# Optimization experiments

Measured on AMD Instinct MI355X. Metric: run time of the kernel, lower is better.

## Reference

```python
import jax, jax.numpy as jnp
import numpy as np

B, IN, E, H, V, MAX_LEN = 512, 64, 512, 1024, 1024, 32
LN_EPS = 1e-5


def setup_inputs() -> dict:
    key = jax.random.key(0)
    ks = jax.random.split(key, 16)
    s = 0.02
    n = lambda k, shp: jax.random.normal(k, shp, jnp.float32) * s
    return {
        "x": jax.random.normal(ks[0], (B, IN), jnp.float32),
        "w_in": n(ks[1], (E, IN)), "b_in": jnp.zeros((E,), jnp.float32),
        "w_ih0": n(ks[2], (4 * H, E)), "w_hh0": n(ks[3], (4 * H, H)),
        "b_ih0": jnp.zeros((4 * H,), jnp.float32), "b_hh0": jnp.zeros((4 * H,), jnp.float32),
        "w_ih1": n(ks[4], (4 * H, H)), "w_hh1": n(ks[5], (4 * H, H)),
        "b_ih1": jnp.zeros((4 * H,), jnp.float32), "b_hh1": jnp.zeros((4 * H,), jnp.float32),
        "ln_g": jnp.ones((H,), jnp.float32), "ln_b": jnp.zeros((H,), jnp.float32),
        "w_out": n(ks[6], (V, H)), "b_out": jnp.zeros((V,), jnp.float32),
        "emb": n(ks[7], (V, E)),
    }


def _lstm_cell(x, h, c, w_ih, w_hh, b_ih, b_hh):
    # PyTorch LSTMCell: gates ordered (input, forget, cell, output)
    gates = x @ w_ih.T + h @ w_hh.T + b_ih + b_hh  # [B, 4H]
    i, f, g, o = jnp.split(gates, 4, axis=1)
    i, f, o = jax.nn.sigmoid(i), jax.nn.sigmoid(f), jax.nn.sigmoid(o)
    g = jnp.tanh(g)
    c2 = f * c + i * g
    h2 = o * jnp.tanh(c2)
    return h2, c2


def reference(x, w_in, b_in, w_ih0, w_hh0, b_ih0, b_hh0,
              w_ih1, w_hh1, b_ih1, b_hh1, ln_g, ln_b, w_out, b_out, emb):
    bsz = x.shape[0]
    hid = w_hh0.shape[1]
    inp = x @ w_in.T + b_in  # [B, E]
    z = jnp.zeros((bsz, hid), jnp.float32)
    init = (z, z, z, z, inp)

    def step(carry, _):
        h0, c0, h1, c1, cur = carry
        h0, c0 = _lstm_cell(cur, h0, c0, w_ih0, w_hh0, b_ih0, b_hh0)
        h1, c1 = _lstm_cell(h0, h1, c1, w_ih1, w_hh1, b_ih1, b_hh1)
        mu = jnp.mean(h1, axis=-1, keepdims=True)
        var = jnp.mean((h1 - mu) ** 2, axis=-1, keepdims=True)
        hn = (h1 - mu) / jnp.sqrt(var + LN_EPS) * ln_g + ln_b
        lp = jax.nn.log_softmax(hn @ w_out.T + b_out, axis=-1)  # [B, V]
        ent = -jnp.sum(jnp.exp(lp) * lp, axis=-1)  # [B]
        sym = jnp.argmax(lp, axis=-1)  # eval-mode (deterministic) path
        logprob = jnp.take_along_axis(lp, sym[:, None], axis=1)[:, 0]
        nxt = emb[sym]  # [B, E]
        return (h0, c0, h1, c1, nxt), (sym, logprob, ent)

    _, (seq, logits, ent) = jax.lax.scan(step, init, None, length=MAX_LEN)
    seq, logits, ent = seq.T, logits.T, ent.T  # [B, MAX_LEN]
    zcol_f = jnp.zeros((bsz, 1), jnp.float32)
    zcol_i = jnp.zeros((bsz, 1), seq.dtype)
    seq = jnp.concatenate([seq, zcol_i], axis=1)
    logits = jnp.concatenate([logits, zcol_f], axis=1)
    ent = jnp.concatenate([ent, zcol_f], axis=1)
    return seq, logits, ent
```

## Files before the change

kernel.cpp:

```cpp
#include <hip/hip_runtime.h>
#include <hip/hip_bf16.h>
#include <math.h>

#define BQ   512
#define EDIM 512
#define HDIM 1024
#define VDIM 1024
#define TLEN 32
#define TOUT 33
#define PGS  (BQ * 4 * HDIM)
#define PLS  (BQ * VDIM)

typedef _Float16 half8  __attribute__((ext_vector_type(8)));
typedef _Float16 half4v __attribute__((ext_vector_type(4)));
typedef float    f32x16 __attribute__((ext_vector_type(16)));

#define GLOAD_LDS16(gp, lp) __builtin_amdgcn_global_load_lds( \
    (const __attribute__((address_space(1))) void*)(gp),      \
    (__attribute__((address_space(3))) void*)(lp), 16, 0, 0)

__device__ __forceinline__ size_t packoff(int r, int k, int K) {
    return (size_t)(r >> 5) * (size_t)(32 * K) + (size_t)(k >> 4) * 512
         + (size_t)((k >> 3) & 1) * 256 + (size_t)(r & 31) * 8 + (size_t)(k & 7);
}

__device__ _Float16 g_curh[BQ*EDIM], g_curl[BQ*EDIM];
__device__ _Float16 g_h0h[BQ*HDIM], g_h0l[BQ*HDIM];
__device__ _Float16 g_h1h[BQ*HDIM], g_h1l[BQ*HDIM];
__device__ _Float16 g_hnh[BQ*HDIM], g_hnl[BQ*HDIM];
__device__ float    g_c0[BQ*HDIM], g_c1[BQ*HDIM];

__device__ _Float16 g_wih0h[4*HDIM*EDIM], g_wih0l[4*HDIM*EDIM];
__device__ _Float16 g_whh0h[4*HDIM*HDIM], g_whh0l[4*HDIM*HDIM];
__device__ _Float16 g_wih1h[4*HDIM*HDIM], g_wih1l[4*HDIM*HDIM];
__device__ _Float16 g_whh1h[4*HDIM*HDIM], g_whh1l[4*HDIM*HDIM];
__device__ _Float16 g_wouth[VDIM*HDIM],   g_woutl[VDIM*HDIM];

__device__ float g_part_g[2 * PGS];
__device__ float g_part_lg[8 * PLS];
__device__ float g_bsum0[4*HDIM], g_bsum1[4*HDIM];

__global__ void init_kernel(float* __restrict__ out,
                            const float* __restrict__ bi0, const float* __restrict__ bh0,
                            const float* __restrict__ bi1, const float* __restrict__ bh1) {
    int i = blockIdx.x * 256 + threadIdx.x;
    g_c0[i] = 0.f; g_c1[i] = 0.f;
    g_h0h[i] = (_Float16)0.f; g_h0l[i] = (_Float16)0.f;
    g_h1h[i] = (_Float16)0.f; g_h1l[i] = (_Float16)0.f;
    if (i < 4 * HDIM) {
        g_bsum0[i] = bi0[i] + bh0[i];
        g_bsum1[i] = bi1[i] + bh1[i];
    }
    if (i < 3 * BQ) {
        int which = i / BQ, b = i % BQ;
        out[(size_t)which * BQ * TOUT + (size_t)b * TOUT + (TOUT - 1)] = 0.f;
    }
}

__global__ void split_pack_kernel(const float* __restrict__ w, _Float16* __restrict__ hi,
                                  _Float16* __restrict__ lo, int klog, int nquads) {
    int q = blockIdx.x * 256 + threadIdx.x;
    if (q >= nquads) return;
    int e = q * 4;
    int r = e >> klog, k = e & ((1 << klog) - 1);
    float4 v = ((const float4*)w)[q];
    half4v h, l;
    h[0] = (_Float16)v.x; l[0] = (_Float16)((v.x - (float)h[0]) * 4096.f);
    h[1] = (_Float16)v.y; l[1] = (_Float16)((v.y - (float)h[1]) * 4096.f);
    h[2] = (_Float16)v.z; l[2] = (_Float16)((v.z - (float)h[2]) * 4096.f);
    h[3] = (_Float16)v.w; l[3] = (_Float16)((v.w - (float)h[3]) * 4096.f);
    size_t po = packoff(r, k, 1 << klog);
    *(half4v*)&hi[po] = h;
    *(half4v*)&lo[po] = l;
}

__device__ __forceinline__ void split1(float x, _Float16* hp, _Float16* lp) {
    _Float16 h = (_Float16)x;
    *hp = h;
    *lp = (_Float16)((x - (float)h) * 4096.f);
}

__global__ __launch_bounds__(256, 2) void gemm_f16split(
    const _Float16* __restrict__ Ah1, const _Float16* __restrict__ Al1, int K1,
    const _Float16* __restrict__ Wh1, const _Float16* __restrict__ Wl1,
    const _Float16* __restrict__ Ah2, const _Float16* __restrict__ Al2, int K2,
    const _Float16* __restrict__ Wh2, const _Float16* __restrict__ Wl2,
    float* __restrict__ outp, int N, int S)
{
    __shared__ __align__(16) _Float16 sA[2][2][2][2][512];
    int tid = threadIdx.x;
    int l = tid & 63, w = tid >> 6;
    int n0 = blockIdx.x * 128, m0 = blockIdx.y * 64, s = blockIdx.z;

    int kch1 = K1 / S, kch2 = K2 / S;
    int n1 = kch1 >> 5, n2 = kch2 >> 5;
    int nit = n1 + n2;

    f32x16 accM0 = {}, accM1 = {}, accL0 = {}, accL1 = {};
    int lr = l & 31, lq = l >> 5;

    auto stageA = [&](int it, int bb) {
        const _Float16 *AhP, *AlP; int K, k0;
        if (it < n1) { AhP = Ah1; AlP = Al1; K = K1; k0 = s * kch1 + it * 32; }
        else         { AhP = Ah2; AlP = Al2; K = K2; k0 = s * kch2 + (it - n1) * 32; }
        #pragma unroll
        for (int qq = 0; qq < 2; ++qq) {
            int q = w * 2 + qq;
            int pl = q >> 2, mh = (q >> 1) & 1, kh = q & 1;
            const _Float16* sp = pl ? AlP : AhP;
            size_t off = (size_t)((m0 >> 5) + mh) * (size_t)(32 * K)
                       + (size_t)((k0 >> 4) + kh) * 512 + (size_t)l * 8;
            GLOAD_LDS16(sp + off, &sA[bb][pl][mh][kh][0]);
        }
    };

    auto loadB = [&](int it, half8 (&Bh)[2], half8 (&Bl)[2]) {
        const _Float16 *WhP, *WlP; int K, k0;
        if (it < n1) { WhP = Wh1; WlP = Wl1; K = K1; k0 = s * kch1 + it * 32; }
        else         { WhP = Wh2; WlP = Wl2; K = K2; k0 = s * kch2 + (it - n1) * 32; }
        size_t strip = (size_t)((n0 >> 5) + w) * (size_t)(32 * K);
        #pragma unroll
        for (int kh = 0; kh < 2; ++kh) {
            size_t off = strip + (size_t)((k0 >> 4) + kh) * 512 + (size_t)l * 8;
            Bh[kh] = *(const half8*)(WhP + off);
            Bl[kh] = *(const half8*)(WlP + off);
        }
    };

    auto compute = [&](int bb, half8 (&Bh)[2], half8 (&Bl)[2]) {
        #pragma unroll
        for (int kh = 0; kh < 2; ++kh) {
            half8 ah0 = *(const half8*)&sA[bb][0][0][kh][(size_t)l * 8];
            half8 ah1 = *(const half8*)&sA[bb][0][1][kh][(size_t)l * 8];
            half8 al0 = *(const half8*)&sA[bb][1][0][kh][(size_t)l * 8];
            half8 al1 = *(const half8*)&sA[bb][1][1][kh][(size_t)l * 8];
            accM0 = __builtin_amdgcn_mfma_f32_32x32x16_f16(ah0, Bh[kh], accM0, 0, 0, 0);
            accM1 = __builtin_amdgcn_mfma_f32_32x32x16_f16(ah1, Bh[kh], accM1, 0, 0, 0);
            accL0 = __builtin_amdgcn_mfma_f32_32x32x16_f16(ah0, Bl[kh], accL0, 0, 0, 0);
            accL1 = __builtin_amdgcn_mfma_f32_32x32x16_f16(ah1, Bl[kh], accL1, 0, 0, 0);
            accL0 = __builtin_amdgcn_mfma_f32_32x32x16_f16(al0, Bh[kh], accL0, 0, 0, 0);
            accL1 = __builtin_amdgcn_mfma_f32_32x32x16_f16(al1, Bh[kh], accL1, 0, 0, 0);
        }
    };

    half8 B0h[2], B0l[2], B1h[2], B1l[2];
    stageA(0, 0);
    loadB(0, B0h, B0l);
    __syncthreads();

    for (int itp = 0; itp < nit; itp += 2) {
        if (itp + 1 < nit) { stageA(itp + 1, 1); loadB(itp + 1, B1h, B1l); }
        compute(0, B0h, B0l);
        __syncthreads();
        if (itp + 2 < nit) { stageA(itp + 2, 0); loadB(itp + 2, B0h, B0l); }
        compute(1, B1h, B1l);
        __syncthreads();
    }

    float* op = outp + (size_t)s * BQ * N;
    int n = n0 + w * 32 + lr;
    #pragma unroll
    for (int r = 0; r < 16; ++r) {
        int row = (r & 3) + 8 * (r >> 2) + 4 * lq;
        op[(size_t)(m0 + row) * N + n]      = accM0[r] + accL0[r] * (1.f / 4096.f);
        op[(size_t)(m0 + 32 + row) * N + n] = accM1[r] + accL1[r] * (1.f / 4096.f);
    }
}

#define GBK 16
#define GPAD 68
__global__ __launch_bounds__(256) void gemm_in(const float* __restrict__ x,
                                               const float* __restrict__ w_in,
                                               const float* __restrict__ b_in) {
    __shared__ __align__(16) float As[GBK][GPAD];
    __shared__ __align__(16) float Bs[GBK][GPAD];
    int tid = threadIdx.x;
    int tx = tid & 15, ty = tid >> 4;
    int m0 = blockIdx.y * 64, n0 = blockIdx.x * 64;
    int lm = tid >> 2, lk = (tid & 3) << 2;
    const int K = 64;
    float acc[4][4] = {};
    for (int k0 = 0; k0 < K; k0 += GBK) {
        float4 av = *(const float4*)(x + (size_t)(m0 + lm) * K + k0 + lk);
        float4 wv = *(const float4*)(w_in + (size_t)(n0 + lm) * K + k0 + lk);
        As[lk + 0][lm] = av.x; As[lk + 1][lm] = av.y;
        As[lk + 2][lm] = av.z; As[lk + 3][lm] = av.w;
        Bs[lk + 0][lm] = wv.x; Bs[lk + 1][lm] = wv.y;
        Bs[lk + 2][lm] = wv.z; Bs[lk + 3][lm] = wv.w;
        __syncthreads();
        #pragma unroll
        for (int kk = 0; kk < GBK; ++kk) {
            float4 a  = *(const float4*)&As[kk][ty * 4];
            float4 bq = *(const float4*)&Bs[kk][tx * 4];
            float aa[4] = {a.x, a.y, a.z, a.w};
            float bb[4] = {bq.x, bq.y, bq.z, bq.w};
            #pragma unroll
            for (int i = 0; i < 4; ++i)
                #pragma unroll
                for (int j = 0; j < 4; ++j)
                    acc[i][j] = fmaf(aa[i], bb[j], acc[i][j]);
        }
        __syncthreads();
    }
    #pragma unroll
    for (int i = 0; i < 4; ++i) {
        int m = m0 + ty * 4 + i;
        int n = n0 + tx * 4;
        half4v h, lo;
        #pragma unroll
        for (int j = 0; j < 4; ++j) {
            float v = acc[i][j] + b_in[n + j];
            _Float16 hv = (_Float16)v;
            h[j] = hv;
            lo[j] = (_Float16)((v - (float)hv) * 4096.f);
        }
        size_t po = packoff(m, n, EDIM);
        *(half4v*)&g_curh[po] = h;
        *(half4v*)&g_curl[po] = lo;
    }
}

__device__ __forceinline__ float sigm(float x) { return 1.f / (1.f + expf(-x)); }

__global__ void lstm0_kernel() {
    int qidx = blockIdx.x * 256 + threadIdx.x;
    int b = qidx >> 8;
    int j = (qidx & 255) * 4;
    size_t base = (size_t)b * 4096;
    float4 G[4];
    #pragma unroll
    for (int g = 0; g < 4; ++g) {
        float4 p0 = *(const float4*)&g_part_g[base + g * 1024 + j];
        float4 p1 = *(const float4*)&g_part_g[PGS + base + g * 1024 + j];
        float4 bs = *(const float4*)&g_bsum0[g * 1024 + j];
        G[g].x = p0.x + p1.x + bs.x;
        G[g].y = p0.y + p1.y + bs.y;
        G[g].z = p0.z + p1.z + bs.z;
        G[g].w = p0.w + p1.w + bs.w;
    }
    size_t hb = (size_t)b * HDIM + j;
    float4 cin = *(const float4*)&g_c0[hb];
    float ci[4] = {cin.x, cin.y, cin.z, cin.w};
    float gi[4] = {G[0].x, G[0].y, G[0].z, G[0].w};
    float gf[4] = {G[1].x, G[1].y, G[1].z, G[1].w};
    float gg[4] = {G[2].x, G[2].y, G[2].z, G[2].w};
    float go[4] = {G[3].x, G[3].y, G[3].z, G[3].w};
    float c[4], h[4];
    half4v hh, hl;
    #pragma unroll
    for (int r = 0; r < 4; ++r) {
        c[r] = sigm(gf[r]) * ci[r] + sigm(gi[r]) * tanhf(gg[r]);
        h[r] = sigm(go[r]) * tanhf(c[r]);
        _Float16 hi16 = (_Float16)h[r];
        hh[r] = hi16;
        hl[r] = (_Float16)((h[r] - (float)hi16) * 4096.f);
    }
    *(float4*)&g_c0[hb] = {c[0], c[1], c[2], c[3]};
    size_t po = packoff(b, j, HDIM);
    *(half4v*)&g_h0h[po] = hh;
    *(half4v*)&g_h0l[po] = hl;
}

__global__ __launch_bounds__(256) void lstm1_ln_kernel(
    const float* __restrict__ ln_g, const float* __restrict__ ln_b)
{
    __shared__ float sbuf[4];
    int b = blockIdx.x, tid = threadIdx.x;
    int lane = tid & 63, wid = tid >> 6;
    int j = tid * 4;
    size_t base = (size_t)b * 4096;
    float4 G[4];
    #pragma unroll
    for (int g = 0; g < 4; ++g) {
        float4 p0 = *(const float4*)&g_part_g[base + g * 1024 + j];
        float4 p1 = *(const float4*)&g_part_g[PGS + base + g * 1024 + j];
        float4 bs = *(const float4*)&g_bsum1[g * 1024 + j];
        G[g].x = p0.x + p1.x + bs.x;
        G[g].y = p0.y + p1.y + bs.y;
        G[g].z = p0.z + p1.z + bs.z;
        G[g].w = p0.w + p1.w + bs.w;
    }
    size_t hb = (size_t)b * HDIM + j;
    float4 cin = *(const float4*)&g_c1[hb];
    float ci[4] = {cin.x, cin.y, cin.z, cin.w};
    float gi[4] = {G[0].x, G[0].y, G[0].z, G[0].w};
    float gf[4] = {G[1].x, G[1].y, G[1].z, G[1].w};
    float gg[4] = {G[2].x, G[2].y, G[2].z, G[2].w};
    float go[4] = {G[3].x, G[3].y, G[3].z, G[3].w};
    float c[4], h[4];
    float sum = 0.f;
    #pragma unroll
    for (int r = 0; r < 4; ++r) {
        c[r] = sigm(gf[r]) * ci[r] + sigm(gi[r]) * tanhf(gg[r]);
        h[r] = sigm(go[r]) * tanhf(c[r]);
        sum += h[r];
    }
    *(float4*)&g_c1[hb] = {c[0], c[1], c[2], c[3]};
    size_t po = packoff(b, j, HDIM);
    half4v h1h, h1l;
    #pragma unroll
    for (int r = 0; r < 4; ++r) {
        _Float16 hi16 = (_Float16)h[r];
        h1h[r] = hi16;
        h1l[r] = (_Float16)((h[r] - (float)hi16) * 4096.f);
    }
    *(half4v*)&g_h1h[po] = h1h;
    *(half4v*)&g_h1l[po] = h1l;

    for (int off = 32; off > 0; off >>= 1) sum += __shfl_down(sum, off, 64);
    if (lane == 0) sbuf[wid] = sum;
    __syncthreads();
    float mu = (sbuf[0] + sbuf[1] + sbuf[2] + sbuf[3]) * (1.f / HDIM);
    __syncthreads();
    float sq = 0.f;
    #pragma unroll
    for (int r = 0; r < 4; ++r) { float d = h[r] - mu; sq += d * d; }
    for (int off = 32; off > 0; off >>= 1) sq += __shfl_down(sq, off, 64);
    if (lane == 0) sbuf[wid] = sq;
    __syncthreads();
    float var = (sbuf[0] + sbuf[1] + sbuf[2] + sbuf[3]) * (1.f / HDIM);
    float rstd = 1.f / sqrtf(var + 1e-5f);
    half4v nh, nl;
    #pragma unroll
    for (int r = 0; r < 4; ++r) {
        float hn = (h[r] - mu) * rstd * ln_g[j + r] + ln_b[j + r];
        _Float16 hi16 = (_Float16)hn;
        nh[r] = hi16;
        nl[r] = (_Float16)((hn - (float)hi16) * 4096.f);
    }
    *(half4v*)&g_hnh[po] = nh;
    *(half4v*)&g_hnl[po] = nl;
}

__global__ __launch_bounds__(256) void softmax_row_kernel(
    const float* __restrict__ b_out, const float* __restrict__ emb,
    float* __restrict__ out, int t)
{
    __shared__ float swv[4];
    __shared__ int   swi[4];
    __shared__ float sZ[4], sS[4];
    __shared__ float s_max;
    __shared__ int   s_idx;
    int b = blockIdx.x, tid = threadIdx.x;
    int lane = tid & 63, wid = tid >> 6;
    size_t base = (size_t)b * VDIM + 4 * tid;
    float4 xv = *(const float4*)&b_out[4 * tid];
    #pragma unroll
    for (int s = 0; s < 8; ++s) {
        float4 p = *(const float4*)&g_part_lg[(size_t)s * PLS + base];
        xv.x += p.x; xv.y += p.y; xv.z += p.z; xv.w += p.w;
    }

    float mv = xv.x; int mi = 4 * tid;
    if (xv.y > mv) { mv = xv.y; mi = 4 * tid + 1; }
    if (xv.z > mv) { mv = xv.z; mi = 4 * tid + 2; }
    if (xv.w > mv) { mv = xv.w; mi = 4 * tid + 3; }
    for (int off = 32; off > 0; off >>= 1) {
        float ov = __shfl_down(mv, off, 64);
        int   oi = __shfl_down(mi, off, 64);
        if (ov > mv || (ov == mv && oi < mi)) { mv = ov; mi = oi; }
    }
    if (lane == 0) { swv[wid] = mv; swi[wid] = mi; }
    __syncthreads();
    if (tid == 0) {
        mv = swv[0]; mi = swi[0];
        for (int w = 1; w < 4; ++w)
            if (swv[w] > mv || (swv[w] == mv && swi[w] < mi)) { mv = swv[w]; mi = swi[w]; }
        s_max = mv; s_idx = mi;
    }
    __syncthreads();
    float xmax = s_max;

    float sv[4] = {xv.x - xmax, xv.y - xmax, xv.z - xmax, xv.w - xmax};
    float z = 0.f, s1 = 0.f;
    #pragma unroll
    for (int r = 0; r < 4; ++r) { float e = expf(sv[r]); z += e; s1 += e * sv[r]; }
    for (int off = 32; off > 0; off >>= 1) {
        z  += __shfl_down(z, off, 64);
        s1 += __shfl_down(s1, off, 64);
    }
    if (lane == 0) { sZ[wid] = z; sS[wid] = s1; }
    __syncthreads();
    if (tid == 0) {
        float Z = sZ[0] + sZ[1] + sZ[2] + sZ[3];
        float S1 = sS[0] + sS[1] + sS[2] + sS[3];
        float logZ = logf(Z);
        float ent = logZ - S1 / Z;
        out[(size_t)b * TOUT + t]                         = (float)s_idx;
        out[(size_t)BQ * TOUT + (size_t)b * TOUT + t]     = -logZ;
        out[(size_t)2 * BQ * TOUT + (size_t)b * TOUT + t] = ent;
    }
    __syncthreads();
    int sym = s_idx;
    const float* e = emb + (size_t)sym * EDIM;
    for (int j = tid; j < EDIM; j += 256) {
        size_t po = packoff(b, j, EDIM);
        split1(e[j], &g_curh[po], &g_curl[po]);
    }
}

extern "C" void kernel_launch(void* const* d_in, const int* in_sizes, int n_in,
                              void* d_out, int out_size, void* d_ws, size_t ws_size,
                              hipStream_t stream) {
    const float* x     = (const float*)d_in[0];
    const float* w_in  = (const float*)d_in[1];
    const float* b_in  = (const float*)d_in[2];
    const float* w_ih0 = (const float*)d_in[3];
    const float* w_hh0 = (const float*)d_in[4];
    const float* b_ih0 = (const float*)d_in[5];
    const float* b_hh0 = (const float*)d_in[6];
    const float* w_ih1 = (const float*)d_in[7];
    const float* w_hh1 = (const float*)d_in[8];
    const float* b_ih1 = (const float*)d_in[9];
    const float* b_hh1 = (const float*)d_in[10];
    const float* ln_g  = (const float*)d_in[11];
    const float* ln_b  = (const float*)d_in[12];
    const float* w_out = (const float*)d_in[13];
    const float* b_out = (const float*)d_in[14];
    const float* emb   = (const float*)d_in[15];
    float* out = (float*)d_out;

    _Float16 *wih0h, *wih0l, *whh0h, *whh0l, *wih1h, *wih1l, *whh1h, *whh1l, *wouth, *woutl;
    hipGetSymbolAddress((void**)&wih0h, HIP_SYMBOL(g_wih0h));
    hipGetSymbolAddress((void**)&wih0l, HIP_SYMBOL(g_wih0l));
    hipGetSymbolAddress((void**)&whh0h, HIP_SYMBOL(g_whh0h));
    hipGetSymbolAddress((void**)&whh0l, HIP_SYMBOL(g_whh0l));
    hipGetSymbolAddress((void**)&wih1h, HIP_SYMBOL(g_wih1h));
    hipGetSymbolAddress((void**)&wih1l, HIP_SYMBOL(g_wih1l));
    hipGetSymbolAddress((void**)&whh1h, HIP_SYMBOL(g_whh1h));
    hipGetSymbolAddress((void**)&whh1l, HIP_SYMBOL(g_whh1l));
    hipGetSymbolAddress((void**)&wouth, HIP_SYMBOL(g_wouth));
    hipGetSymbolAddress((void**)&woutl, HIP_SYMBOL(g_woutl));
    _Float16 *curh, *curl, *h0h, *h0l, *h1h, *h1l, *hnh, *hnl;
    hipGetSymbolAddress((void**)&curh, HIP_SYMBOL(g_curh));
    hipGetSymbolAddress((void**)&curl, HIP_SYMBOL(g_curl));
    hipGetSymbolAddress((void**)&h0h, HIP_SYMBOL(g_h0h));
    hipGetSymbolAddress((void**)&h0l, HIP_SYMBOL(g_h0l));
    hipGetSymbolAddress((void**)&h1h, HIP_SYMBOL(g_h1h));
    hipGetSymbolAddress((void**)&h1l, HIP_SYMBOL(g_h1l));
    hipGetSymbolAddress((void**)&hnh, HIP_SYMBOL(g_hnh));
    hipGetSymbolAddress((void**)&hnl, HIP_SYMBOL(g_hnl));
    float *part_g, *part_lg;
    hipGetSymbolAddress((void**)&part_g, HIP_SYMBOL(g_part_g));
    hipGetSymbolAddress((void**)&part_lg, HIP_SYMBOL(g_part_lg));

    init_kernel<<<(BQ * HDIM) / 256, 256, 0, stream>>>(out, b_ih0, b_hh0, b_ih1, b_hh1);

    split_pack_kernel<<<(4*HDIM*EDIM/4 + 255)/256, 256, 0, stream>>>(w_ih0, wih0h, wih0l, 9,  4*HDIM*EDIM/4);
    split_pack_kernel<<<(4*HDIM*HDIM/4 + 255)/256, 256, 0, stream>>>(w_hh0, whh0h, whh0l, 10, 4*HDIM*HDIM/4);
    split_pack_kernel<<<(4*HDIM*HDIM/4 + 255)/256, 256, 0, stream>>>(w_ih1, wih1h, wih1l, 10, 4*HDIM*HDIM/4);
    split_pack_kernel<<<(4*HDIM*HDIM/4 + 255)/256, 256, 0, stream>>>(w_hh1, whh1h, whh1l, 10, 4*HDIM*HDIM/4);
    split_pack_kernel<<<(VDIM*HDIM/4 + 255)/256, 256, 0, stream>>>(w_out, wouth, woutl, 10, VDIM*HDIM/4);

    gemm_in<<<dim3(EDIM / 64, BQ / 64), 256, 0, stream>>>(x, w_in, b_in);

    for (int t = 0; t < TLEN; ++t) {
        gemm_f16split<<<dim3(4 * HDIM / 128, BQ / 64, 2), 256, 0, stream>>>(
            curh, curl, EDIM, wih0h, wih0l,
            h0h, h0l, HDIM, whh0h, whh0l,
            part_g, 4 * HDIM, 2);
        lstm0_kernel<<<(BQ * HDIM / 4) / 256, 256, 0, stream>>>();

        gemm_f16split<<<dim3(4 * HDIM / 128, BQ / 64, 2), 256, 0, stream>>>(
            h0h, h0l, HDIM, wih1h, wih1l,
            h1h, h1l, HDIM, whh1h, whh1l,
            part_g, 4 * HDIM, 2);
        lstm1_ln_kernel<<<BQ, 256, 0, stream>>>(ln_g, ln_b);

        gemm_f16split<<<dim3(VDIM / 128, BQ / 64, 8), 256, 0, stream>>>(
            hnh, hnl, HDIM, wouth, woutl,
            (const _Float16*)nullptr, (const _Float16*)nullptr, 0,
            (const _Float16*)nullptr, (const _Float16*)nullptr,
            part_lg, VDIM, 8);

        softmax_row_kernel<<<BQ, 256, 0, stream>>>(b_out, emb, out, t);
    }
}
```

Baseline: 2.943 ms.

## Replace LDS-staged split GEMM with register-only 64x64 tiles and XCD-aware block mapping

The split-f16 GEMM no longer stages A through shared memory. Each wave now loads its A and B fragments straight from global memory into registers, with a 4-deep register prefetch, and computes one 32x32 output per wave inside a 64x64 block tile. Block indices are remapped so N-tiles are grouped per XCD, which aims to improve L2 reuse of the weights. The gate GEMMs drop split-K and fold the bias into the epilogue, which removes the partial-sum buffer and its reduction reads in the LSTM kernels. The logits GEMM goes from split-K 8 to 4. The trade-off is that each wave has less reuse, since A is reloaded per wave and not shared through LDS, and register pressure is higher.

```diff
diff --git a/kernel.cpp b/kernel.cpp
--- a/kernel.cpp
+++ b/kernel.cpp
@@ -8,16 +8,11 @@
 #define VDIM 1024
 #define TLEN 32
 #define TOUT 33
-#define PGS  (BQ * 4 * HDIM)
 #define PLS  (BQ * VDIM)
 
 typedef _Float16 half8  __attribute__((ext_vector_type(8)));
 typedef _Float16 half4v __attribute__((ext_vector_type(4)));
 typedef float    f32x16 __attribute__((ext_vector_type(16)));
-
-#define GLOAD_LDS16(gp, lp) __builtin_amdgcn_global_load_lds( \
-    (const __attribute__((address_space(1))) void*)(gp),      \
-    (__attribute__((address_space(3))) void*)(lp), 16, 0, 0)
 
 __device__ __forceinline__ size_t packoff(int r, int k, int K) {
     return (size_t)(r >> 5) * (size_t)(32 * K) + (size_t)(k >> 4) * 512
@@ -36,8 +31,8 @@
 __device__ _Float16 g_whh1h[4*HDIM*HDIM], g_whh1l[4*HDIM*HDIM];
 __device__ _Float16 g_wouth[VDIM*HDIM],   g_woutl[VDIM*HDIM];
 
-__device__ float g_part_g[2 * PGS];
-__device__ float g_part_lg[8 * PLS];
+__device__ float g_gates[BQ * 4 * HDIM];
+__device__ float g_part_lg[4 * PLS];
 __device__ float g_bsum0[4*HDIM], g_bsum1[4*HDIM];
 
 __global__ void init_kernel(float* __restrict__ out,
@@ -80,90 +75,91 @@
     *lp = (_Float16)((x - (float)h) * 4096.f);
 }
 
-__global__ __launch_bounds__(256, 2) void gemm_f16split(
+__global__ __launch_bounds__(256, 2) void gemm_nolds(
     const _Float16* __restrict__ Ah1, const _Float16* __restrict__ Al1, int K1,
     const _Float16* __restrict__ Wh1, const _Float16* __restrict__ Wl1,
     const _Float16* __restrict__ Ah2, const _Float16* __restrict__ Al2, int K2,
     const _Float16* __restrict__ Wh2, const _Float16* __restrict__ Wl2,
-    float* __restrict__ outp, int N, int S)
+    const float* __restrict__ bias, float* __restrict__ outp,
+    int N, int S, int P)
 {
-    __shared__ __align__(16) _Float16 sA[2][2][2][2][512];
     int tid = threadIdx.x;
     int l = tid & 63, w = tid >> 6;
-    int n0 = blockIdx.x * 128, m0 = blockIdx.y * 64, s = blockIdx.z;
+    int lr = l & 31, lq = l >> 5;
+    int mh = w >> 1, nh = w & 1;
+
+    int wb = blockIdx.x;
+    int xcd = wb & 7, q = wb >> 3;
+    int nb = xcd * P + (q % P);
+    int rest = q / P;
+    int s = rest % S;
+    int mb = rest / S;
 
     int kch1 = K1 / S, kch2 = K2 / S;
-    int n1 = kch1 >> 5, n2 = kch2 >> 5;
-    int nit = n1 + n2;
-
-    f32x16 accM0 = {}, accM1 = {}, accL0 = {}, accL1 = {};
-    int lr = l & 31, lq = l >> 5;
-
-    auto stageA = [&](int it, int bb) {
-        const _Float16 *AhP, *AlP; int K, k0;
-        if (it < n1) { AhP = Ah1; AlP = Al1; K = K1; k0 = s * kch1 + it * 32; }
-        else         { AhP = Ah2; AlP = Al2; K = K2; k0 = s * kch2 + (it - n1) * 32; }
-        #pragma unroll
-        for (int qq = 0; qq < 2; ++qq) {
-            int q = w * 2 + qq;
-            int pl = q >> 2, mh = (q >> 1) & 1, kh = q & 1;
-            const _Float16* sp = pl ? AlP : AhP;
-            size_t off = (size_t)((m0 >> 5) + mh) * (size_t)(32 * K)
-                       + (size_t)((k0 >> 4) + kh) * 512 + (size_t)l * 8;
-            GLOAD_LDS16(sp + off, &sA[bb][pl][mh][kh][0]);
-        }
-    };
-
-    auto loadB = [&](int it, half8 (&Bh)[2], half8 (&Bl)[2]) {
-        const _Float16 *WhP, *WlP; int K, k0;
-        if (it < n1) { WhP = Wh1; WlP = Wl1; K = K1; k0 = s * kch1 + it * 32; }
-        else         { WhP = Wh2; WlP = Wl2; K = K2; k0 = s * kch2 + (it - n1) * 32; }
-        size_t strip = (size_t)((n0 >> 5) + w) * (size_t)(32 * K);
-        #pragma unroll
-        for (int kh = 0; kh < 2; ++kh) {
-            size_t off = strip + (size_t)((k0 >> 4) + kh) * 512 + (size_t)l * 8;
-            Bh[kh] = *(const half8*)(WhP + off);
-            Bl[kh] = *(const half8*)(WlP + off);
-        }
-    };
-
-    auto compute = [&](int bb, half8 (&Bh)[2], half8 (&Bl)[2]) {
-        #pragma unroll
-        for (int kh = 0; kh < 2; ++kh) {
-            half8 ah0 = *(const half8*)&sA[bb][0][0][kh][(size_t)l * 8];
-            half8 ah1 = *(const half8*)&sA[bb][0][1][kh][(size_t)l * 8];
-            half8 al0 = *(const half8*)&sA[bb][1][0][kh][(size_t)l * 8];
-            half8 al1 = *(const half8*)&sA[bb][1][1][kh][(size_t)l * 8];
-            accM0 = __builtin_amdgcn_mfma_f32_32x32x16_f16(ah0, Bh[kh], accM0, 0, 0, 0);
-            accM1 = __builtin_amdgcn_mfma_f32_32x32x16_f16(ah1, Bh[kh], accM1, 0, 0, 0);
-            accL0 = __builtin_amdgcn_mfma_f32_32x32x16_f16(ah0, Bl[kh], accL0, 0, 0, 0);
-            accL1 = __builtin_amdgcn_mfma_f32_32x32x16_f16(ah1, Bl[kh], accL1, 0, 0, 0);
-            accL0 = __builtin_amdgcn_mfma_f32_32x32x16_f16(al0, Bh[kh], accL0, 0, 0, 0);
-            accL1 = __builtin_amdgcn_mfma_f32_32x32x16_f16(al1, Bh[kh], accL1, 0, 0, 0);
-        }
-    };
-
-    half8 B0h[2], B0l[2], B1h[2], B1l[2];
-    stageA(0, 0);
-    loadB(0, B0h, B0l);
-    __syncthreads();
-
-    for (int itp = 0; itp < nit; itp += 2) {
-        if (itp + 1 < nit) { stageA(itp + 1, 1); loadB(itp + 1, B1h, B1l); }
-        compute(0, B0h, B0l);
-        __syncthreads();
-        if (itp + 2 < nit) { stageA(itp + 2, 0); loadB(itp + 2, B0h, B0l); }
-        compute(1, B1h, B1l);
-        __syncthreads();
-    }
-
+    int n1 = kch1 >> 5;
+    int nit = n1 + (kch2 >> 5);
+
+    size_t aoff1 = (size_t)(mb*2+mh) * (size_t)(32*K1) + (size_t)((s*kch1) >> 4) * 512 + (size_t)l*8;
+    size_t boff1 = (size_t)(nb*2+nh) * (size_t)(32*K1) + (size_t)((s*kch1) >> 4) * 512 + (size_t)l*8;
+    const _Float16* pAh1 = Ah1 + aoff1;
+    const _Float16* pAl1 = Al1 + aoff1;
+    const _Float16* pWh1 = Wh1 + boff1;
+    const _Float16* pWl1 = Wl1 + boff1;
+    const _Float16 *pAh2 = pAh1, *pAl2 = pAl1, *pWh2 = pWh1, *pWl2 = pWl1;
+    if (K2 > 0) {
+        size_t aoff2 = (size_t)(mb*2+mh) * (size_t)(32*K2) + (size_t)((s*kch2) >> 4) * 512 + (size_t)l*8;
+        size_t boff2 = (size_t)(nb*2+nh) * (size_t)(32*K2) + (size_t)((s*kch2) >> 4) * 512 + (size_t)l*8;
+        pAh2 = Ah2 + aoff2; pAl2 = Al2 + aoff2;
+        pWh2 = Wh2 + boff2; pWl2 = Wl2 + boff2;
+    }
+
+    f32x16 accM = {}, accL = {};
+
+#define LOAD_IT(it, A, B) { \
+        int it_ = (it); size_t off_; \
+        const _Float16 *ah_, *al_, *wh_, *wl_; \
+        if (it_ < n1) { off_ = (size_t)it_ * 1024;        ah_ = pAh1; al_ = pAl1; wh_ = pWh1; wl_ = pWl1; } \
+        else          { off_ = (size_t)(it_ - n1) * 1024; ah_ = pAh2; al_ = pAl2; wh_ = pWh2; wl_ = pWl2; } \
+        A[0][0] = *(const half8*)(ah_ + off_);       A[0][1] = *(const half8*)(ah_ + off_ + 512); \
+        A[1][0] = *(const half8*)(al_ + off_);       A[1][1] = *(const half8*)(al_ + off_ + 512); \
+        B[0][0] = *(const half8*)(wh_ + off_);       B[0][1] = *(const half8*)(wh_ + off_ + 512); \
+        B[1][0] = *(const half8*)(wl_ + off_);       B[1][1] = *(const half8*)(wl_ + off_ + 512); \
+    }
+
+#define COMP_IT(A, B) { \
+        _Pragma("unroll") \
+        for (int kh_ = 0; kh_ < 2; ++kh_) { \
+            accM = __builtin_amdgcn_mfma_f32_32x32x16_f16(A[0][kh_], B[0][kh_], accM, 0, 0, 0); \
+            accL = __builtin_amdgcn_mfma_f32_32x32x16_f16(A[0][kh_], B[1][kh_], accL, 0, 0, 0); \
+            accL = __builtin_amdgcn_mfma_f32_32x32x16_f16(A[1][kh_], B[0][kh_], accL, 0, 0, 0); \
+        } \
+    }
+
+    half8 A0[2][2], B0[2][2], A1[2][2], B1[2][2];
+    half8 A2[2][2], B2[2][2], A3[2][2], B3[2][2];
+    LOAD_IT(0, A0, B0);
+    LOAD_IT(1, A1, B1);
+    for (int itp = 0; itp < nit; itp += 4) {
+        if (itp + 2 < nit) LOAD_IT(itp + 2, A2, B2);
+        COMP_IT(A0, B0);
+        if (itp + 3 < nit) LOAD_IT(itp + 3, A3, B3);
+        COMP_IT(A1, B1);
+        if (itp + 4 < nit) LOAD_IT(itp + 4, A0, B0);
+        COMP_IT(A2, B2);
+        if (itp + 5 < nit) LOAD_IT(itp + 5, A1, B1);
+        COMP_IT(A3, B3);
+    }
+#undef LOAD_IT
+#undef COMP_IT
+
+    int n = nb * 64 + nh * 32 + lr;
+    int m0 = mb * 64 + mh * 32;
+    float bv = bias ? bias[n] : 0.f;
     float* op = outp + (size_t)s * BQ * N;
-    int n = n0 + w * 32 + lr;
     #pragma unroll
     for (int r = 0; r < 16; ++r) {
         int row = (r & 3) + 8 * (r >> 2) + 4 * lq;
-        op[(size_t)(m0 + row) * N + n]      = accM0[r] + accL0[r] * (1.f / 4096.f);
-        op[(size_t)(m0 + 32 + row) * N + n] = accM1[r] + accL1[r] * (1.f / 4096.f);
+        op[(size_t)(m0 + row) * N + n] = accM[r] + accL[r] * (1.f / 4096.f) + bv;
     }
 }
 
@@ -229,15 +225,7 @@
     size_t base = (size_t)b * 4096;
     float4 G[4];
     #pragma unroll
-    for (int g = 0; g < 4; ++g) {
-        float4 p0 = *(const float4*)&g_part_g[base + g * 1024 + j];
-        float4 p1 = *(const float4*)&g_part_g[PGS + base + g * 1024 + j];
-        float4 bs = *(const float4*)&g_bsum0[g * 1024 + j];
-        G[g].x = p0.x + p1.x + bs.x;
-        G[g].y = p0.y + p1.y + bs.y;
-        G[g].z = p0.z + p1.z + bs.z;
-        G[g].w = p0.w + p1.w + bs.w;
-    }
+    for (int g = 0; g < 4; ++g) G[g] = *(const float4*)&g_gates[base + g * 1024 + j];
     size_t hb = (size_t)b * HDIM + j;
     float4 cin = *(const float4*)&g_c0[hb];
     float ci[4] = {cin.x, cin.y, cin.z, cin.w};
@@ -271,15 +259,7 @@
     size_t base = (size_t)b * 4096;
     float4 G[4];
     #pragma unroll
-    for (int g = 0; g < 4; ++g) {
-        float4 p0 = *(const float4*)&g_part_g[base + g * 1024 + j];
-        float4 p1 = *(const float4*)&g_part_g[PGS + base + g * 1024 + j];
-        float4 bs = *(const float4*)&g_bsum1[g * 1024 + j];
-        G[g].x = p0.x + p1.x + bs.x;
-        G[g].y = p0.y + p1.y + bs.y;
-        G[g].z = p0.z + p1.z + bs.z;
-        G[g].w = p0.w + p1.w + bs.w;
-    }
+    for (int g = 0; g < 4; ++g) G[g] = *(const float4*)&g_gates[base + g * 1024 + j];
     size_t hb = (size_t)b * HDIM + j;
     float4 cin = *(const float4*)&g_c1[hb];
     float ci[4] = {cin.x, cin.y, cin.z, cin.w};
@@ -346,7 +326,7 @@
     size_t base = (size_t)b * VDIM + 4 * tid;
     float4 xv = *(const float4*)&b_out[4 * tid];
     #pragma unroll
-    for (int s = 0; s < 8; ++s) {
+    for (int s = 0; s < 4; ++s) {
         float4 p = *(const float4*)&g_part_lg[(size_t)s * PLS + base];
         xv.x += p.x; xv.y += p.y; xv.z += p.z; xv.w += p.w;
     }
@@ -440,9 +420,11 @@
     hipGetSymbolAddress((void**)&h1l, HIP_SYMBOL(g_h1l));
     hipGetSymbolAddress((void**)&hnh, HIP_SYMBOL(g_hnh));
     hipGetSymbolAddress((void**)&hnl, HIP_SYMBOL(g_hnl));
-    float *part_g, *part_lg;
-    hipGetSymbolAddress((void**)&part_g, HIP_SYMBOL(g_part_g));
+    float *gates, *part_lg, *bsum0, *bsum1;
+    hipGetSymbolAddress((void**)&gates, HIP_SYMBOL(g_gates));
     hipGetSymbolAddress((void**)&part_lg, HIP_SYMBOL(g_part_lg));
+    hipGetSymbolAddress((void**)&bsum0, HIP_SYMBOL(g_bsum0));
+    hipGetSymbolAddress((void**)&bsum1, HIP_SYMBOL(g_bsum1));
 
     init_kernel<<<(BQ * HDIM) / 256, 256, 0, stream>>>(out, b_ih0, b_hh0, b_ih1, b_hh1);
 
@@ -455,23 +437,23 @@
     gemm_in<<<dim3(EDIM / 64, BQ / 64), 256, 0, stream>>>(x, w_in, b_in);
 
     for (int t = 0; t < TLEN; ++t) {
-        gemm_f16split<<<dim3(4 * HDIM / 128, BQ / 64, 2), 256, 0, stream>>>(
+        gemm_nolds<<<512, 256, 0, stream>>>(
             curh, curl, EDIM, wih0h, wih0l,
             h0h, h0l, HDIM, whh0h, whh0l,
-            part_g, 4 * HDIM, 2);
+            bsum0, gates, 4 * HDIM, 1, 8);
         lstm0_kernel<<<(BQ * HDIM / 4) / 256, 256, 0, stream>>>();
 
-        gemm_f16split<<<dim3(4 * HDIM / 128, BQ / 64, 2), 256, 0, stream>>>(
+        gemm_nolds<<<512, 256, 0, stream>>>(
             h0h, h0l, HDIM, wih1h, wih1l,
             h1h, h1l, HDIM, whh1h, whh1l,
-            part_g, 4 * HDIM, 2);
+            bsum1, gates, 4 * HDIM, 1, 8);
         lstm1_ln_kernel<<<BQ, 256, 0, stream>>>(ln_g, ln_b);
 
-        gemm_f16split<<<dim3(VDIM / 128, BQ / 64, 8), 256, 0, stream>>>(
+        gemm_nolds<<<512, 256, 0, stream>>>(
             hnh, hnl, HDIM, wouth, woutl,
             (const _Float16*)nullptr, (const _Float16*)nullptr, 0,
             (const _Float16*)nullptr, (const _Float16*)nullptr,
-            part_lg, VDIM, 8);
+            (const float*)nullptr, part_lg, VDIM, 4, 2);
 
         softmax_row_kernel<<<BQ, 256, 0, stream>>>(b_out, emb, out, t);
     }
```

After: 3.234 ms. 1.1x slower.
